# Kernel tuning notes

Measured on AMD Instinct MI355X. Metric: run time of the kernel, lower is better.

The kernel has to match this reference:

```python
import jax, jax.numpy as jnp
from jax import lax
import numpy as np

HID = 128            # hidden_dim
DILS = (1, 3, 9, 27) # dilations (used only by the dense dilated convs)
CONV_SIZE = 3        # dilated conv kernel size
KER = 3              # LVC kernel size
SLOPE = 0.2          # lReLU slope after preconv
BLOCK_SLOPE = float(KER)  # NOTE: source passes ker_size into LVC_ConvBlock's slope arg
COND = 512           # cond channels


def setup_inputs() -> dict:
    key = jax.random.key(0)
    ks = jax.random.split(key, 12)
    B, T, Lc = 4, 32768, 128  # hop_size = T // Lc = 256
    nl = len(DILS)
    f = lambda k, s: jax.random.normal(k, s, dtype=jnp.float32) * 0.02
    return {
        "x": jax.random.normal(ks[0], (B, 1, T), dtype=jnp.float32),
        "c": jax.random.normal(ks[1], (B, COND, Lc), dtype=jnp.float32),
        # KernelPredictor 1x1 convs (weight-normed at init == plain weights)
        "kernel_w": f(ks[2], (HID * HID * KER * nl, COND)),
        "kernel_b": f(ks[3], (HID * HID * KER * nl,)),
        "biasp_w": f(ks[4], (HID * nl, COND)),
        "biasp_b": f(ks[5], (HID * nl,)),
        "pre_w": f(ks[6], (HID, 1)),
        "pre_b": f(ks[7], (HID,)),
        "block_w": f(ks[8], (nl, HID, HID, CONV_SIZE)),
        "block_b": f(ks[9], (nl, HID)),
        "post_w": f(ks[10], (1, HID)),
        "post_b": f(ks[11], (1,)),
    }


def _leaky(x, s):
    return jnp.where(x >= 0, x, s * x)


def _conv1x1(x, w, b):  # x: (B,C,T), w: (O,C), b: (O,)
    return jnp.einsum('oc,bct->bot', w, x) + b[:, None]


def _dilconv(x, w, b, d):  # x: (B,C,T), w: (O,I,K)
    pad = d * (CONV_SIZE - 1) // 2
    y = lax.conv_general_dilated(x, w, window_strides=(1,), padding=[(pad, pad)],
                                 rhs_dilation=(d,), dimension_numbers=('NCH', 'OIH', 'NCH'))
    return y + b[:, None]


def _lvc(x, kernel, bias, hop):
    # x: (B,C,T); kernel: (B,C,O,K,L); bias: (B,O,L). dilation=1 (as in source call).
    B, C, T = x.shape
    O, K, L = kernel.shape[2], kernel.shape[3], kernel.shape[4]
    p = (K - 1) // 2
    xp = jnp.pad(x, ((0, 0), (0, 0), (p, p)))
    # stride-1 sliding windows of width K, grouped into L hop-blocks of size hop
    win = jnp.stack([xp[:, :, j:j + T] for j in range(K)], axis=-1)  # (B,C,T,K)
    win = win.reshape(B, C, L, hop, K)
    o = jnp.einsum('bilsk,biokl->bols', win, kernel) + bias[:, :, :, None]
    return o.reshape(B, O, T)


def reference(x, c, kernel_w, kernel_b, biasp_w, biasp_b, pre_w, pre_b,
              block_w, block_b, post_w, post_b):
    B, _, T = x.shape
    Lc = c.shape[-1]
    nl = len(DILS)
    hop = T // Lc
    # kernel predictor: view order (B, layers, in, out, K, L)
    k_all = _conv1x1(c, kernel_w, kernel_b).reshape(B, nl, HID, HID, KER, Lc)
    b_all = _conv1x1(c, biasp_w, biasp_b).reshape(B, nl, HID, Lc)
    h = _leaky(_conv1x1(x, pre_w, pre_b), SLOPE)
    for i, d in enumerate(DILS):
        h = _lvc(h, k_all[:, i], b_all[:, i], hop)
        h = _leaky(h, BLOCK_SLOPE)
        h = _dilconv(h, block_w[i], block_b[i], d)
        h = _leaky(h, BLOCK_SLOPE)
    return _conv1x1(h, post_w, post_b)
```

## Files before the change

kernel.cpp:

```cpp
#include <hip/hip_runtime.h>

#define T_LEN 32768
#define HIDC  128
#define LC    128
#define HOP   256
#define CONDC 512
#define NLAY  4
#define MROWS 49152

typedef __attribute__((ext_vector_type(8))) short short8;
typedef __attribute__((ext_vector_type(4))) float f32x4;

static __device__ __forceinline__ unsigned short f2b(float f) {
  union { float f; unsigned u; } v; v.f = f;
  unsigned r = v.u + 0x7FFFu + ((v.u >> 16) & 1u);
  return (unsigned short)(r >> 16);
}
static __device__ __forceinline__ float b2f(unsigned short h) {
  union { unsigned u; float f; } v; v.u = ((unsigned)h) << 16;
  return v.f;
}


__global__ void k_cbt(const float* __restrict__ c, unsigned short* __restrict__ cbt) {
  int idx = blockIdx.x * 256 + threadIdx.x;
  int n = idx >> 9, ch = idx & 511;
  int b = n >> 7, l = n & 127;
  cbt[idx] = f2b(c[(size_t)(b * CONDC + ch) * LC + l]);
}

__global__ void k_bwt(const float* __restrict__ bw, unsigned short* __restrict__ bwt) {
  int idx = blockIdx.x * 256 + threadIdx.x;
  int i = idx & 127, o = (idx >> 7) & 127, kl = idx >> 14;
  int k = kl % 3, layer = kl / 3;
  bwt[idx] = f2b(bw[((size_t)(layer * HIDC + o) * HIDC + i) * 3 + k]);
}

__global__ void k_bias(const float* __restrict__ c, const float* __restrict__ bw,
                       const float* __restrict__ bb, float* __restrict__ ball) {
  int m = blockIdx.x, b = blockIdx.y, l = threadIdx.x;
  const float* crow = c + (size_t)b * CONDC * LC + l;
  const float* wrow = bw + (size_t)m * CONDC;
  float acc = 0.f;
  for (int ch = 0; ch < CONDC; ++ch) acc = fmaf(wrow[ch], crow[(size_t)ch * LC], acc);
  int layer = m >> 7, o = m & 127;
  ball[((size_t)(b * NLAY + layer) * HIDC + o) * LC + l] = acc + bb[m];
}

__global__ void k_pre(const float* __restrict__ x, const float* __restrict__ pw,
                      const float* __restrict__ pb, unsigned short* __restrict__ h) {
  int idx = blockIdx.x * 256 + threadIdx.x;
  int o4 = (idx & 31) << 2;
  int bt = idx >> 5;
  float xv = x[bt];
  float4 w = *(const float4*)(pw + o4);
  float4 bi = *(const float4*)(pb + o4);
  float r0 = fmaf(w.x, xv, bi.x); r0 = r0 >= 0.f ? r0 : 0.2f * r0;
  float r1 = fmaf(w.y, xv, bi.y); r1 = r1 >= 0.f ? r1 : 0.2f * r1;
  float r2 = fmaf(w.z, xv, bi.z); r2 = r2 >= 0.f ? r2 : 0.2f * r2;
  float r3 = fmaf(w.w, xv, bi.w); r3 = r3 >= 0.f ? r3 : 0.2f * r3;
  ushort4 s; s.x = f2b(r0); s.y = f2b(r1); s.z = f2b(r2); s.w = f2b(r3);
  *(ushort4*)(h + (size_t)bt * HIDC + o4) = s;
}

__global__ void k_post(const unsigned short* __restrict__ h, const float* __restrict__ pw,
                       const float* __restrict__ pb, float* __restrict__ out) {
  int t = blockIdx.x * 256 + threadIdx.x;
  const unsigned short* r = h + (size_t)t * HIDC;
  float acc = 0.f;
#pragma unroll
  for (int o = 0; o < HIDC; o += 8) {
    int4 w = *(const int4*)(r + o);
    int ws_[4] = {w.x, w.y, w.z, w.w};
#pragma unroll
    for (int j = 0; j < 4; ++j) {
      unsigned v = (unsigned)ws_[j];
      acc = fmaf(b2f((unsigned short)(v & 0xFFFFu)), pw[o + j * 2], acc);
      acc = fmaf(b2f((unsigned short)(v >> 16)),     pw[o + j * 2 + 1], acc);
    }
  }
  out[t] = acc + pb[0];
}

__global__ __launch_bounds__(256) void k_kpred(
    const float* __restrict__ A, const float* __restrict__ bias,
    const unsigned short* __restrict__ Bt, unsigned short* __restrict__ C) {
  __shared__ __align__(16) unsigned short As[128 * 72];
  __shared__ __align__(16) unsigned short Bs[128 * 72];
  const int mtile = blockIdx.x * 128;
  const int oc = (blockIdx.x & 127) * 3 + (blockIdx.x >> 7);
  const int ntile = blockIdx.y * 128;
  const int tid = threadIdx.x;
  const int wave = tid >> 6, lane = tid & 63;
  const int wm = (wave & 1) * 64, wn = (wave >> 1) * 64;
  const int lm = lane & 15, quad = lane >> 4;
  f32x4 acc[4][4] = {};
  for (int k0 = 0; k0 < CONDC; k0 += 64) {
#pragma unroll
    for (int it = 0; it < 8; ++it) {
      int idx = it * 256 + tid;
      int row = idx >> 4, kq = (idx & 15) << 2;
      float4 v = *(const float4*)(A + ((size_t)row * 384 + oc) * CONDC + k0 + kq);
      ushort4 s; s.x = f2b(v.x); s.y = f2b(v.y); s.z = f2b(v.z); s.w = f2b(v.w);
      *(ushort4*)(&As[row * 72 + kq]) = s;
    }
#pragma unroll
    for (int it = 0; it < 4; ++it) {
      int idx = it * 256 + tid;
      int row = idx >> 3, k8 = (idx & 7) << 3;
      *(int4*)(&Bs[row * 72 + k8]) = *(const int4*)(Bt + (size_t)(ntile + row) * CONDC + k0 + k8);
    }
    __syncthreads();
#pragma unroll
    for (int kk = 0; kk < 2; ++kk) {
      short8 af[4], bf[4];
#pragma unroll
      for (int mb = 0; mb < 4; ++mb)
        af[mb] = *(const short8*)(&As[(wm + mb * 16 + lm) * 72 + kk * 32 + quad * 8]);
#pragma unroll
      for (int nb = 0; nb < 4; ++nb)
        bf[nb] = *(const short8*)(&Bs[(wn + nb * 16 + lm) * 72 + kk * 32 + quad * 8]);
#pragma unroll
      for (int mb = 0; mb < 4; ++mb)
#pragma unroll
        for (int nb = 0; nb < 4; ++nb)
          acc[mb][nb] = __builtin_amdgcn_mfma_f32_16x16x32_bf16(af[mb], bf[nb], acc[mb][nb], 0, 0, 0);
    }
    __syncthreads();
  }
#pragma unroll
  for (int mb = 0; mb < 4; ++mb) {
    int i0 = wm + mb * 16 + quad * 4;
    int m0 = mtile + i0;
    float b0 = bias[(size_t)i0 * 384 + oc];
    float b1 = bias[(size_t)(i0 + 1) * 384 + oc];
    float b2 = bias[(size_t)(i0 + 2) * 384 + oc];
    float b3 = bias[(size_t)(i0 + 3) * 384 + oc];
#pragma unroll
    for (int nb = 0; nb < 4; ++nb) {
      int n = ntile + wn + nb * 16 + lm;
      f32x4 v = acc[mb][nb];
      ushort4 s;
      s.x = f2b(v.x + b0); s.y = f2b(v.y + b1); s.z = f2b(v.z + b2); s.w = f2b(v.w + b3);
      *(ushort4*)(&C[(size_t)n * MROWS + m0]) = s;
    }
  }
}

__global__ __launch_bounds__(512) void k_lvc(
    const unsigned short* __restrict__ hin, const unsigned short* __restrict__ kbuf,
    const float* __restrict__ ball, unsigned short* __restrict__ hout, int layer) {
  __shared__ __align__(16) unsigned short Hs[258 * 40];
  __shared__ __align__(16) unsigned short As[3 * 128 * 40];
  const int l = blockIdx.x, b = blockIdx.y;
  const int t0 = l * HOP;
  const int tid = threadIdx.x;
  const int wave = tid >> 6, lane = tid & 63;
  const int wm = (wave & 1) * 64, wn = (wave >> 1) * 64;
  const int lm = lane & 15, quad = lane >> 4;
  const unsigned short* hb = hin + (size_t)b * T_LEN * HIDC;
  const unsigned short* kb = kbuf + (size_t)(b * LC + l) * MROWS;
  f32x4 acc[4][4] = {};
  for (int ic = 0; ic < HIDC; ic += 32) {
    __syncthreads();
#pragma unroll
    for (int p = 0; p < 3; ++p) {
      int idx = p * 512 + tid;
      if (idx < 258 * 4) {
        int u = idx >> 2, i8 = (idx & 3) << 3;
        int t = t0 + u - 1;
        int4 v = {0, 0, 0, 0};
        if (t >= 0 && t < T_LEN) v = *(const int4*)(hb + (size_t)t * HIDC + ic + i8);
        *(int4*)(&Hs[u * 40 + i8]) = v;
      }
    }
#pragma unroll
    for (int p = 0; p < 3; ++p) {
      int idx = p * 512 + tid;
      int ko = idx >> 2, i8 = (idx & 3) << 3;
      *(int4*)(&As[ko * 40 + i8]) = *(const int4*)(kb + (size_t)ko * HIDC + ic + i8);
    }
    __syncthreads();
#pragma unroll
    for (int k = 0; k < 3; ++k) {
      short8 af[4], bf[4];
#pragma unroll
      for (int mb = 0; mb < 4; ++mb)
        af[mb] = *(const short8*)(&As[(k * 128 + wm + mb * 16 + lm) * 40 + quad * 8]);
#pragma unroll
      for (int nb = 0; nb < 4; ++nb)
        bf[nb] = *(const short8*)(&Hs[(wn + nb * 16 + lm + k) * 40 + quad * 8]);
#pragma unroll
      for (int mb = 0; mb < 4; ++mb)
#pragma unroll
        for (int nb = 0; nb < 4; ++nb)
          acc[mb][nb] = __builtin_amdgcn_mfma_f32_16x16x32_bf16(af[mb], bf[nb], acc[mb][nb], 0, 0, 0);
    }
  }
  const float* bp = ball + (size_t)(b * NLAY + layer) * HIDC * LC + l;
#pragma unroll
  for (int mb = 0; mb < 4; ++mb) {
    int o0 = wm + mb * 16 + quad * 4;
    float bi[4];
#pragma unroll
    for (int j = 0; j < 4; ++j) bi[j] = bp[(size_t)(o0 + j) * LC];
#pragma unroll
    for (int nb = 0; nb < 4; ++nb) {
      int s = wn + nb * 16 + lm;
      f32x4 v = acc[mb][nb];
      float r0 = v.x + bi[0]; r0 = r0 >= 0.f ? r0 : 3.f * r0;
      float r1 = v.y + bi[1]; r1 = r1 >= 0.f ? r1 : 3.f * r1;
      float r2 = v.z + bi[2]; r2 = r2 >= 0.f ? r2 : 3.f * r2;
      float r3 = v.w + bi[3]; r3 = r3 >= 0.f ? r3 : 3.f * r3;
      ushort4 st; st.x = f2b(r0); st.y = f2b(r1); st.z = f2b(r2); st.w = f2b(r3);
      *(ushort4*)(&hout[((size_t)b * T_LEN + t0 + s) * HIDC + o0]) = st;
    }
  }
}

__global__ __launch_bounds__(512) void k_dconv(
    const unsigned short* __restrict__ hin, const unsigned short* __restrict__ bwt,
    const float* __restrict__ bb, unsigned short* __restrict__ hout, int d) {
  __shared__ __align__(16) unsigned short Hs[310 * 40];
  __shared__ __align__(16) unsigned short As[3 * 128 * 40];
  const int tb = blockIdx.x * HOP, b = blockIdx.y;
  const int U4 = (HOP + 2 * d) * 4;
  const int tid = threadIdx.x;
  const int wave = tid >> 6, lane = tid & 63;
  const int wm = (wave & 1) * 64, wn = (wave >> 1) * 64;
  const int lm = lane & 15, quad = lane >> 4;
  const unsigned short* hb = hin + (size_t)b * T_LEN * HIDC;
  f32x4 acc[4][4] = {};
  for (int ic = 0; ic < HIDC; ic += 32) {
    __syncthreads();
#pragma unroll
    for (int p = 0; p < 3; ++p) {
      int idx = p * 512 + tid;
      if (idx < U4) {
        int u = idx >> 2, i8 = (idx & 3) << 3;
        int t = tb + u - d;
        int4 v = {0, 0, 0, 0};
        if (t >= 0 && t < T_LEN) v = *(const int4*)(hb + (size_t)t * HIDC + ic + i8);
        *(int4*)(&Hs[u * 40 + i8]) = v;
      }
    }
#pragma unroll
    for (int p = 0; p < 3; ++p) {
      int idx = p * 512 + tid;
      int ko = idx >> 2, i8 = (idx & 3) << 3;
      *(int4*)(&As[ko * 40 + i8]) = *(const int4*)(bwt + (size_t)ko * HIDC + ic + i8);
    }
    __syncthreads();
#pragma unroll
    for (int k = 0; k < 3; ++k) {
      short8 af[4], bf[4];
#pragma unroll
      for (int mb = 0; mb < 4; ++mb)
        af[mb] = *(const short8*)(&As[(k * 128 + wm + mb * 16 + lm) * 40 + quad * 8]);
#pragma unroll
      for (int nb = 0; nb < 4; ++nb)
        bf[nb] = *(const short8*)(&Hs[(wn + nb * 16 + lm + k * d) * 40 + quad * 8]);
#pragma unroll
      for (int mb = 0; mb < 4; ++mb)
#pragma unroll
        for (int nb = 0; nb < 4; ++nb)
          acc[mb][nb] = __builtin_amdgcn_mfma_f32_16x16x32_bf16(af[mb], bf[nb], acc[mb][nb], 0, 0, 0);
    }
  }
#pragma unroll
  for (int mb = 0; mb < 4; ++mb) {
    int o0 = wm + mb * 16 + quad * 4;
    float bi[4];
#pragma unroll
    for (int j = 0; j < 4; ++j) bi[j] = bb[o0 + j];
#pragma unroll
    for (int nb = 0; nb < 4; ++nb) {
      int s = wn + nb * 16 + lm;
      f32x4 v = acc[mb][nb];
      float r0 = v.x + bi[0]; r0 = r0 >= 0.f ? r0 : 3.f * r0;
      float r1 = v.y + bi[1]; r1 = r1 >= 0.f ? r1 : 3.f * r1;
      float r2 = v.z + bi[2]; r2 = r2 >= 0.f ? r2 : 3.f * r2;
      float r3 = v.w + bi[3]; r3 = r3 >= 0.f ? r3 : 3.f * r3;
      ushort4 st; st.x = f2b(r0); st.y = f2b(r1); st.z = f2b(r2); st.w = f2b(r3);
      *(ushort4*)(&hout[((size_t)b * T_LEN + tb + s) * HIDC + o0]) = st;
    }
  }
}

extern "C" void kernel_launch(void* const* d_in, const int* in_sizes, int n_in,
                              void* d_out, int out_size, void* d_ws, size_t ws_size,
                              hipStream_t stream) {
  const float* x        = (const float*)d_in[0];
  const float* c        = (const float*)d_in[1];
  const float* kernel_w = (const float*)d_in[2];
  const float* kernel_b = (const float*)d_in[3];
  const float* biasp_w  = (const float*)d_in[4];
  const float* biasp_b  = (const float*)d_in[5];
  const float* pre_w    = (const float*)d_in[6];
  const float* pre_b    = (const float*)d_in[7];
  const float* block_w  = (const float*)d_in[8];
  const float* block_b  = (const float*)d_in[9];
  const float* post_w   = (const float*)d_in[10];
  const float* post_b   = (const float*)d_in[11];
  float* out = (float*)d_out;

  char* ws = (char*)d_ws;
  unsigned short* h0   = (unsigned short*)ws;
  unsigned short* h1   = (unsigned short*)(ws + 33554432);
  unsigned short* kbuf = (unsigned short*)(ws + 67108864);
  float*          ball = (float*)(ws + 117440512);
  unsigned short* cbt  = (unsigned short*)(ws + 118489088);
  unsigned short* bwt  = (unsigned short*)(ws + 119013376);

  k_cbt<<<1024, 256, 0, stream>>>(c, cbt);
  k_bwt<<<768, 256, 0, stream>>>(block_w, bwt);
  k_bias<<<dim3(512, 4), 128, 0, stream>>>(c, biasp_w, biasp_b, ball);
  k_pre<<<16384, 256, 0, stream>>>(x, pre_w, pre_b, h0);

  unsigned short* cur = h0;
  unsigned short* nxt = h1;
  const int dils[4] = {1, 3, 9, 27};
  for (int layer = 0; layer < 4; ++layer) {
    k_kpred<<<dim3(384, 4), 256, 0, stream>>>(kernel_w + (size_t)layer * MROWS * CONDC,
                                              kernel_b + (size_t)layer * MROWS, cbt, kbuf);
    k_lvc<<<dim3(128, 4), 512, 0, stream>>>(cur, kbuf, ball, nxt, layer);
    unsigned short* t = cur; cur = nxt; nxt = t;
    k_dconv<<<dim3(128, 4), 512, 0, stream>>>(cur, bwt + (size_t)layer * 3 * HIDC * HIDC,
                                              block_b + layer * HIDC, nxt, dils[layer]);
    t = cur; cur = nxt; nxt = t;
  }
  k_post<<<512, 256, 0, stream>>>(cur, post_w, post_b, out);
}
```

Measured before the change: 1.051 ms.

## Retile kernel-predictor GEMM so each block covers full N, reading weights once

Changes k_kpred tiling from 128x128 tiles over a 4-wide N grid to 64-row tiles that span all 512 output columns. Each fp32 weight row is then loaded and converted to bf16 once instead of four times, cutting the dominant global-memory traffic. In exchange the small cbt operand is reloaded per block from L2. Per-wave accumulators grow to 32 MFMA tiles, which raises register pressure, and the K step shrinks to 32, adding more barriers per block.

After: 1.084 ms. 1.03x slower.

```diff
diff --git a/kernel.cpp b/kernel.cpp
--- a/kernel.cpp
+++ b/kernel.cpp
@@ -82,63 +82,61 @@
   out[t] = acc + pb[0];
 }
 
-__global__ __launch_bounds__(256) void k_kpred(
+__global__ __launch_bounds__(256, 2) void k_kpred(
     const float* __restrict__ A, const float* __restrict__ bias,
     const unsigned short* __restrict__ Bt, unsigned short* __restrict__ C) {
-  __shared__ __align__(16) unsigned short As[128 * 72];
-  __shared__ __align__(16) unsigned short Bs[128 * 72];
-  const int mtile = blockIdx.x * 128;
-  const int oc = (blockIdx.x & 127) * 3 + (blockIdx.x >> 7);
-  const int ntile = blockIdx.y * 128;
+  __shared__ __align__(16) unsigned short As[64 * 40];
+  __shared__ __align__(16) unsigned short Bs[512 * 40];
+  const int bx = blockIdx.x;
+  const int oc = ((bx >> 1) & 127) * 3 + (bx >> 8);
+  const int i0 = (bx & 1) * 64;
+  const int m0g = bx * 64;
   const int tid = threadIdx.x;
   const int wave = tid >> 6, lane = tid & 63;
-  const int wm = (wave & 1) * 64, wn = (wave >> 1) * 64;
+  const int wn = wave * 128;
   const int lm = lane & 15, quad = lane >> 4;
-  f32x4 acc[4][4] = {};
-  for (int k0 = 0; k0 < CONDC; k0 += 64) {
+  f32x4 acc[4][8] = {};
+  for (int k0 = 0; k0 < CONDC; k0 += 32) {
+#pragma unroll
+    for (int it = 0; it < 2; ++it) {
+      int idx = it * 256 + tid;
+      int row = idx >> 3, kq = (idx & 7) << 2;
+      float4 v = *(const float4*)(A + ((size_t)(i0 + row) * 384 + oc) * CONDC + k0 + kq);
+      ushort4 s; s.x = f2b(v.x); s.y = f2b(v.y); s.z = f2b(v.z); s.w = f2b(v.w);
+      *(ushort4*)(&As[row * 40 + kq]) = s;
+    }
 #pragma unroll
     for (int it = 0; it < 8; ++it) {
       int idx = it * 256 + tid;
-      int row = idx >> 4, kq = (idx & 15) << 2;
-      float4 v = *(const float4*)(A + ((size_t)row * 384 + oc) * CONDC + k0 + kq);
-      ushort4 s; s.x = f2b(v.x); s.y = f2b(v.y); s.z = f2b(v.z); s.w = f2b(v.w);
-      *(ushort4*)(&As[row * 72 + kq]) = s;
-    }
-#pragma unroll
-    for (int it = 0; it < 4; ++it) {
-      int idx = it * 256 + tid;
-      int row = idx >> 3, k8 = (idx & 7) << 3;
-      *(int4*)(&Bs[row * 72 + k8]) = *(const int4*)(Bt + (size_t)(ntile + row) * CONDC + k0 + k8);
-    }
-    __syncthreads();
-#pragma unroll
-    for (int kk = 0; kk < 2; ++kk) {
-      short8 af[4], bf[4];
-#pragma unroll
-      for (int mb = 0; mb < 4; ++mb)
-        af[mb] = *(const short8*)(&As[(wm + mb * 16 + lm) * 72 + kk * 32 + quad * 8]);
-#pragma unroll
-      for (int nb = 0; nb < 4; ++nb)
-        bf[nb] = *(const short8*)(&Bs[(wn + nb * 16 + lm) * 72 + kk * 32 + quad * 8]);
-#pragma unroll
-      for (int mb = 0; mb < 4; ++mb)
-#pragma unroll
-        for (int nb = 0; nb < 4; ++nb)
-          acc[mb][nb] = __builtin_amdgcn_mfma_f32_16x16x32_bf16(af[mb], bf[nb], acc[mb][nb], 0, 0, 0);
-    }
+      int row = idx >> 2, k8 = (idx & 3) << 3;
+      *(int4*)(&Bs[row * 40 + k8]) = *(const int4*)(Bt + (size_t)row * CONDC + k0 + k8);
+    }
+    __syncthreads();
+    short8 af[4], bf[8];
+#pragma unroll
+    for (int mb = 0; mb < 4; ++mb)
+      af[mb] = *(const short8*)(&As[(mb * 16 + lm) * 40 + quad * 8]);
+#pragma unroll
+    for (int nb = 0; nb < 8; ++nb)
+      bf[nb] = *(const short8*)(&Bs[(wn + nb * 16 + lm) * 40 + quad * 8]);
+#pragma unroll
+    for (int mb = 0; mb < 4; ++mb)
+#pragma unroll
+      for (int nb = 0; nb < 8; ++nb)
+        acc[mb][nb] = __builtin_amdgcn_mfma_f32_16x16x32_bf16(af[mb], bf[nb], acc[mb][nb], 0, 0, 0);
     __syncthreads();
   }
 #pragma unroll
   for (int mb = 0; mb < 4; ++mb) {
-    int i0 = wm + mb * 16 + quad * 4;
-    int m0 = mtile + i0;
-    float b0 = bias[(size_t)i0 * 384 + oc];
-    float b1 = bias[(size_t)(i0 + 1) * 384 + oc];
-    float b2 = bias[(size_t)(i0 + 2) * 384 + oc];
-    float b3 = bias[(size_t)(i0 + 3) * 384 + oc];
-#pragma unroll
-    for (int nb = 0; nb < 4; ++nb) {
-      int n = ntile + wn + nb * 16 + lm;
+    int ii = i0 + mb * 16 + quad * 4;
+    int m0 = m0g + mb * 16 + quad * 4;
+    float b0 = bias[(size_t)ii * 384 + oc];
+    float b1 = bias[(size_t)(ii + 1) * 384 + oc];
+    float b2 = bias[(size_t)(ii + 2) * 384 + oc];
+    float b3 = bias[(size_t)(ii + 3) * 384 + oc];
+#pragma unroll
+    for (int nb = 0; nb < 8; ++nb) {
+      int n = wn + nb * 16 + lm;
       f32x4 v = acc[mb][nb];
       ushort4 s;
       s.x = f2b(v.x + b0); s.y = f2b(v.y + b1); s.z = f2b(v.z + b2); s.w = f2b(v.w + b3);
@@ -321,8 +319,8 @@
   unsigned short* nxt = h1;
   const int dils[4] = {1, 3, 9, 27};
   for (int layer = 0; layer < 4; ++layer) {
-    k_kpred<<<dim3(384, 4), 256, 0, stream>>>(kernel_w + (size_t)layer * MROWS * CONDC,
-                                              kernel_b + (size_t)layer * MROWS, cbt, kbuf);
+    k_kpred<<<768, 256, 0, stream>>>(kernel_w + (size_t)layer * MROWS * CONDC,
+                                     kernel_b + (size_t)layer * MROWS, cbt, kbuf);
     k_lvc<<<dim3(128, 4), 512, 0, stream>>>(cur, kbuf, ball, nxt, layer);
     unsigned short* t = cur; cur = nxt; nxt = t;
     k_dconv<<<dim3(128, 4), 512, 0, stream>>>(cur, bwt + (size_t)layer * 3 * HIDC * HIDC,
```
